# Optimization experiments

Measured on AMD Instinct MI355X. Metric: run time of the kernel, lower is better.

The kernel has to match this reference:

```python
import jax, jax.numpy as jnp
import numpy as np

N = 50000          # nodes
E = 800000         # edges (avg degree 16)
D = 128            # feature dim
MSG_EPS = 1e-7     # GENConv eps added to relu(msg)
SM_EPS = 1e-16     # pyg softmax denominator eps
BN_EPS = 1e-5
LN_EPS = 1e-5


def setup_inputs() -> dict:
    key = jax.random.key(0)
    ks = jax.random.split(key, 6)
    x = jax.random.normal(ks[0], (N, D), dtype=jnp.float32)
    edge_index = jax.random.randint(ks[1], (2, E), 0, N, dtype=jnp.int32)
    t = jnp.array(1.0, dtype=jnp.float32)
    W1 = jax.random.normal(ks[2], (D, 2 * D), dtype=jnp.float32) / np.sqrt(D).astype(np.float32)
    b1 = jnp.zeros((2 * D,), jnp.float32)
    bn_gamma = jnp.ones((2 * D,), jnp.float32)
    bn_beta = jnp.zeros((2 * D,), jnp.float32)
    W2 = jax.random.normal(ks[3], (2 * D, D), dtype=jnp.float32) / np.sqrt(2 * D).astype(np.float32)
    b2 = jnp.zeros((D,), jnp.float32)
    ln_gamma = jnp.ones((D,), jnp.float32)
    ln_beta = jnp.zeros((D,), jnp.float32)
    return {"x": x, "edge_index": edge_index, "t": t, "W1": W1, "b1": b1,
            "bn_gamma": bn_gamma, "bn_beta": bn_beta, "W2": W2, "b2": b2,
            "ln_gamma": ln_gamma, "ln_beta": ln_beta}


def reference(x, edge_index, t, W1, b1, bn_gamma, bn_beta, W2, b2, ln_gamma, ln_beta):
    src, dst = edge_index[0], edge_index[1]
    # --- GENConv message: relu(x_j) + eps  -> [E, D]
    msg = jax.nn.relu(x[src]) + MSG_EPS
    # --- softmax aggregation over incoming edges per dst node, per feature
    logits = t * msg                                            # [E, D]
    seg_max = jax.ops.segment_max(logits, dst, num_segments=N)  # [N, D]
    seg_max = jnp.where(jnp.isfinite(seg_max), seg_max, 0.0)    # empty segments -> 0
    ex = jnp.exp(logits - seg_max[dst])                         # [E, D]
    denom = jax.ops.segment_sum(ex, dst, num_segments=N)        # [N, D]
    alpha = ex / (denom[dst] + SM_EPS)                          # [E, D]
    agg = jax.ops.segment_sum(alpha * msg, dst, num_segments=N) # [N, D]
    # --- GENConv update: MLP(agg + x), MLP = Lin(D,2D)->BN->ReLU->Lin(2D,D)
    h = agg + x
    h = h @ W1 + b1                                             # [N, 2D]
    mu = jnp.mean(h, axis=0)
    var = jnp.var(h, axis=0)
    h = (h - mu) * jax.lax.rsqrt(var + BN_EPS) * bn_gamma + bn_beta
    h = jax.nn.relu(h)
    h = h @ W2 + b2                                             # [N, D]
    # --- LayerNorm -> ReLU -> (dropout p=0 noop) -> residual
    mu2 = jnp.mean(h, axis=-1, keepdims=True)
    var2 = jnp.mean(jnp.square(h - mu2), axis=-1, keepdims=True)
    h = (h - mu2) * jax.lax.rsqrt(var2 + LN_EPS) * ln_gamma + ln_beta
    h = jax.nn.relu(h)
    return x + h
```

## Files before the change

kernel.cpp:

```cpp
#include <hip/hip_runtime.h>

#define D 128
#define D2 256
#define BSH 6
#define BNODES 64
#define NBMAX 1024
#define CAP 1280
#define PCHUNK 4096

typedef __attribute__((ext_vector_type(8))) short short8;
typedef __attribute__((ext_vector_type(4))) float f32x4;

__device__ inline unsigned short f2b(float f) {
  unsigned u = __float_as_uint(f);
  unsigned r = (u + 0x7FFFu + ((u >> 16) & 1u)) >> 16;
  return (unsigned short)r;
}
__device__ inline float b2f(unsigned short h) {
  return __uint_as_float(((unsigned)h) << 16);
}

__global__ void convert_w_kernel(const float* __restrict__ W1,
                                 const float* __restrict__ W2,
                                 unsigned short* __restrict__ W1f,
                                 unsigned short* __restrict__ W2f) {
  int idx = blockIdx.x * 256 + threadIdx.x;
  if (idx < 32768) {
    int k = idx >> 8, n = idx & 255;
    int t = n >> 4, m16 = n & 15;
    int kk = k >> 5, quad = (k >> 3) & 3, j = k & 7;
    W1f[(((t * 4 + kk) * 64 + quad * 16 + m16) << 3) + j] = f2b(W1[idx]);
  } else {
    int i = idx - 32768;
    int k = i >> 7, n = i & 127;
    int t = n >> 4, m16 = n & 15;
    int kk = k >> 5, quad = (k >> 3) & 3, j = k & 7;
    W2f[(((t * 8 + kk) * 64 + quad * 16 + m16) << 3) + j] = f2b(W2[i]);
  }
}

__global__ void mb_kernel(const float* __restrict__ x, unsigned short* __restrict__ mb,
                          int total4) {
  int i = blockIdx.x * 256 + threadIdx.x;
  if (i >= total4) return;
  float4 v = reinterpret_cast<const float4*>(x)[i];
  unsigned lo = (unsigned)f2b(fmaxf(v.x, 0.f) + 1e-7f) |
                ((unsigned)f2b(fmaxf(v.y, 0.f) + 1e-7f) << 16);
  unsigned hi = (unsigned)f2b(fmaxf(v.z, 0.f) + 1e-7f) |
                ((unsigned)f2b(fmaxf(v.w, 0.f) + 1e-7f) << 16);
  reinterpret_cast<uint2*>(mb)[i] = make_uint2(lo, hi);
}

__global__ __launch_bounds__(256) void part_kernel(const int* __restrict__ ei,
                                                   int* __restrict__ cursor,
                                                   unsigned* __restrict__ pairbuf,
                                                   int E, int nb) {
  __shared__ int cnt[NBMAX];
  __shared__ int base[NBMAX];
  int tid = threadIdx.x;
  int c0 = blockIdx.x * PCHUNK;
  int nE = min(PCHUNK, E - c0);
  for (int i = tid; i < nb; i += 256) cnt[i] = 0;
  __syncthreads();
  for (int j = tid; j < nE; j += 256) {
    int dst = ei[E + c0 + j];
    atomicAdd(&cnt[dst >> BSH], 1);
  }
  __syncthreads();
  for (int i = tid; i < nb; i += 256) {
    int c = cnt[i];
    base[i] = (c > 0) ? atomicAdd(&cursor[i], c) : 0;
    cnt[i] = 0;
  }
  __syncthreads();
  for (int j = tid; j < nE; j += 256) {
    int e = c0 + j;
    int dst = ei[E + e];
    int src = ei[e];
    int b = dst >> BSH;
    int r = base[b] + atomicAdd(&cnt[b], 1);
    if (r < CAP)
      pairbuf[(size_t)b * CAP + r] =
          (unsigned)src | ((unsigned)(dst & (BNODES - 1)) << 16);
  }
}

__global__ __launch_bounds__(512) void agg2_kernel(const float* __restrict__ x,
                                                   const unsigned short* __restrict__ mb,
                                                   const unsigned* __restrict__ pairbuf,
                                                   const int* __restrict__ cursor,
                                                   const float* __restrict__ tptr,
                                                   unsigned short* __restrict__ h0b, int N) {
  __shared__ unsigned spair[CAP];
  __shared__ unsigned short ssrc[CAP];
  __shared__ int cnt[BNODES], off[BNODES], run[BNODES];
  int b = blockIdx.x;
  int tid = threadIdx.x;
  int Eb = min(cursor[b], CAP);
  if (tid < BNODES) { cnt[tid] = 0; run[tid] = 0; }
  __syncthreads();
  for (int j = tid; j < Eb; j += 512) {
    unsigned p = pairbuf[(size_t)b * CAP + j];
    spair[j] = p;
    atomicAdd(&cnt[p >> 16], 1);
  }
  __syncthreads();
  if (tid < 64) {
    int v = cnt[tid];
    int s = v;
#pragma unroll
    for (int st = 1; st < 64; st <<= 1) {
      int u = __shfl_up(s, st, 64);
      if (tid >= st) s += u;
    }
    off[tid] = s - v;
  }
  __syncthreads();
  for (int j = tid; j < Eb; j += 512) {
    unsigned p = spair[j];
    int dl = p >> 16;
    int r = atomicAdd(&run[dl], 1);
    ssrc[off[dl] + r] = (unsigned short)(p & 0xffffu);
  }
  __syncthreads();

  int w = tid >> 6;
  int l = tid & 63;
  float t = tptr[0];
  const unsigned short* mbc = mb + 2 * l;
  for (int ln = w; ln < BNODES; ln += 8) {
    int n = (b << BSH) + ln;
    if (n >= N) continue;
    int s0 = off[ln];
    int dn = cnt[ln];
    float den0 = 0.f, num0 = 0.f, den1 = 0.f, num1 = 0.f;
    int j = 0;
    for (; j + 8 <= dn; j += 8) {
      unsigned uu[8];
#pragma unroll
      for (int q = 0; q < 8; ++q) {
        int aq = ssrc[s0 + j + q];
        uu[q] = *reinterpret_cast<const unsigned*>(mbc + ((size_t)aq << 7));
      }
#pragma unroll
      for (int q = 0; q < 8; ++q) {
        float m0 = b2f((unsigned short)(uu[q] & 0xffffu));
        float m1 = b2f((unsigned short)(uu[q] >> 16));
        float e0 = __expf(t * m0);
        float e1 = __expf(t * m1);
        den0 += e0; num0 += e0 * m0;
        den1 += e1; num1 += e1 * m1;
      }
    }
    for (; j < dn; ++j) {
      int aq = ssrc[s0 + j];
      unsigned u = *reinterpret_cast<const unsigned*>(mbc + ((size_t)aq << 7));
      float m0 = b2f((unsigned short)(u & 0xffffu));
      float m1 = b2f((unsigned short)(u >> 16));
      float e0 = __expf(t * m0);
      float e1 = __expf(t * m1);
      den0 += e0; num0 += e0 * m0;
      den1 += e1; num1 += e1 * m1;
    }
    size_t idx = ((size_t)n << 7) + 2 * l;
    float2 xv = *reinterpret_cast<const float2*>(x + idx);
    float v0 = num0 / (den0 + 1e-16f) + xv.x;
    float v1 = num1 / (den1 + 1e-16f) + xv.y;
    *reinterpret_cast<unsigned*>(h0b + idx) =
        (unsigned)f2b(v0) | ((unsigned)f2b(v1) << 16);
  }
}

__global__ __launch_bounds__(256) void gemm1_mfma(
    const unsigned short* __restrict__ h0b, const unsigned short* __restrict__ W1f,
    const float* __restrict__ b1, unsigned short* __restrict__ h1b,
    float* __restrict__ bnsum, float* __restrict__ bnsumsq, int M) {
  int tid = threadIdx.x;
  int w = tid >> 6;
  int l = tid & 63;
  int m16 = l & 15;
  int quad = l >> 4;
  int r0 = blockIdx.x * 64;

  f32x4 acc[4][4];
#pragma unroll
  for (int rt = 0; rt < 4; ++rt)
#pragma unroll
    for (int ct = 0; ct < 4; ++ct) acc[rt][ct] = (f32x4){0.f, 0.f, 0.f, 0.f};

#pragma unroll
  for (int kk = 0; kk < 4; ++kk) {
    short8 bfr[4];
#pragma unroll
    for (int ct = 0; ct < 4; ++ct)
      bfr[ct] = *reinterpret_cast<const short8*>(
          W1f + ((((w * 4 + ct) * 4 + kk) * 64 + l) << 3));
    short8 a[4];
#pragma unroll
    for (int rt = 0; rt < 4; ++rt) {
      int row = min(r0 + rt * 16 + m16, M - 1);
      a[rt] = *reinterpret_cast<const short8*>(h0b + (size_t)row * D + kk * 32 + quad * 8);
    }
#pragma unroll
    for (int rt = 0; rt < 4; ++rt)
#pragma unroll
      for (int ct = 0; ct < 4; ++ct)
        acc[rt][ct] = __builtin_amdgcn_mfma_f32_16x16x32_bf16(a[rt], bfr[ct], acc[rt][ct], 0, 0, 0);
  }

#pragma unroll
  for (int ct = 0; ct < 4; ++ct) {
    int col = w * 64 + ct * 16 + m16;
    float bv = b1[col];
    float cs = 0.f, cq = 0.f;
#pragma unroll
    for (int rt = 0; rt < 4; ++rt) {
      int rowb = r0 + rt * 16 + quad * 4;
#pragma unroll
      for (int reg = 0; reg < 4; ++reg) {
        int row = rowb + reg;
        float val = acc[rt][ct][reg] + bv;
        if (row < M) {
          cs += val;
          cq += val * val;
          h1b[(size_t)row * D2 + col] = f2b(val);
        }
      }
    }
    cs += __shfl_xor(cs, 16, 64);
    cs += __shfl_xor(cs, 32, 64);
    cq += __shfl_xor(cq, 16, 64);
    cq += __shfl_xor(cq, 32, 64);
    if (quad == 0) {
      atomicAdd(&bnsum[col], cs);
      atomicAdd(&bnsumsq[col], cq);
    }
  }
}

__global__ void bnfinal_kernel(const float* __restrict__ bnsum,
                               const float* __restrict__ bnsumsq,
                               const float* __restrict__ gamma,
                               const float* __restrict__ beta,
                               float* __restrict__ scale,
                               float* __restrict__ shift, int M) {
  int c = threadIdx.x;
  float invM = 1.f / (float)M;
  float mu = bnsum[c] * invM;
  float var = bnsumsq[c] * invM - mu * mu;
  float sc = gamma[c] * rsqrtf(var + 1e-5f);
  scale[c] = sc;
  shift[c] = beta[c] - mu * sc;
}

__global__ __launch_bounds__(256) void gemm2_mfma(
    const unsigned short* __restrict__ h1b, const unsigned short* __restrict__ W2f,
    const float* __restrict__ b2, const float* __restrict__ bnscale,
    const float* __restrict__ bnshift, const float* __restrict__ lng,
    const float* __restrict__ lnb, const float* __restrict__ x,
    float* __restrict__ out, int M) {
  __shared__ float lnp[128][2], lnp2[128][2];
  int tid = threadIdx.x;
  int w = tid >> 6;
  int l = tid & 63;
  int m16 = l & 15;
  int quad = l >> 4;
  int rb = w >> 1, cb = w & 1;
  int r00 = blockIdx.x * 128;

  f32x4 acc[4][4];
#pragma unroll
  for (int rt = 0; rt < 4; ++rt)
#pragma unroll
    for (int ct = 0; ct < 4; ++ct) acc[rt][ct] = (f32x4){0.f, 0.f, 0.f, 0.f};

#pragma unroll
  for (int kk = 0; kk < 8; ++kk) {
    int c0 = kk * 32 + quad * 8;
    f32x4 sc0 = *reinterpret_cast<const f32x4*>(bnscale + c0);
    f32x4 sc1 = *reinterpret_cast<const f32x4*>(bnscale + c0 + 4);
    f32x4 sh0 = *reinterpret_cast<const f32x4*>(bnshift + c0);
    f32x4 sh1 = *reinterpret_cast<const f32x4*>(bnshift + c0 + 4);
    short8 a[4];
#pragma unroll
    for (int rt = 0; rt < 4; ++rt) {
      int row = min(r00 + rb * 64 + rt * 16 + m16, M - 1);
      short8 raw = *reinterpret_cast<const short8*>(h1b + (size_t)row * D2 + kk * 32 + quad * 8);
#pragma unroll
      for (int j = 0; j < 4; ++j) {
        a[rt][j] = (short)f2b(fmaxf(b2f((unsigned short)raw[j]) * sc0[j] + sh0[j], 0.f));
        a[rt][j + 4] = (short)f2b(fmaxf(b2f((unsigned short)raw[j + 4]) * sc1[j] + sh1[j], 0.f));
      }
    }
    short8 bfr[4];
#pragma unroll
    for (int ct = 0; ct < 4; ++ct)
      bfr[ct] = *reinterpret_cast<const short8*>(
          W2f + ((((cb * 4 + ct) * 8 + kk) * 64 + l) << 3));
#pragma unroll
    for (int rt = 0; rt < 4; ++rt)
#pragma unroll
      for (int ct = 0; ct < 4; ++ct)
        acc[rt][ct] = __builtin_amdgcn_mfma_f32_16x16x32_bf16(a[rt], bfr[ct], acc[rt][ct], 0, 0, 0);
  }

  float b2v[4], lgv[4], lbv[4];
#pragma unroll
  for (int ct = 0; ct < 4; ++ct) {
    int col = cb * 64 + ct * 16 + m16;
    b2v[ct] = b2[col];
    lgv[ct] = lng[col];
    lbv[ct] = lnb[col];
  }

#pragma unroll
  for (int rt = 0; rt < 4; ++rt) {
#pragma unroll
    for (int reg = 0; reg < 4; ++reg) {
      float s = 0.f, s2 = 0.f;
#pragma unroll
      for (int ct = 0; ct < 4; ++ct) {
        float v = acc[rt][ct][reg] + b2v[ct];
        s += v;
        s2 += v * v;
      }
#pragma unroll
      for (int msk = 1; msk < 16; msk <<= 1) {
        s += __shfl_xor(s, msk, 64);
        s2 += __shfl_xor(s2, msk, 64);
      }
      if (m16 == 0) {
        int rl = rb * 64 + rt * 16 + quad * 4 + reg;
        lnp[rl][cb] = s;
        lnp2[rl][cb] = s2;
      }
    }
  }
  __syncthreads();

#pragma unroll
  for (int rt = 0; rt < 4; ++rt) {
#pragma unroll
    for (int reg = 0; reg < 4; ++reg) {
      int rl = rb * 64 + rt * 16 + quad * 4 + reg;
      int row = r00 + rl;
      float s = lnp[rl][0] + lnp[rl][1];
      float s2 = lnp2[rl][0] + lnp2[rl][1];
      float mu = s * (1.f / 128.f);
      float var = s2 * (1.f / 128.f) - mu * mu;
      float inv = rsqrtf(var + 1e-5f);
      if (row < M) {
#pragma unroll
        for (int ct = 0; ct < 4; ++ct) {
          int col = cb * 64 + ct * 16 + m16;
          float v = acc[rt][ct][reg] + b2v[ct];
          float h = fmaxf((v - mu) * inv * lgv[ct] + lbv[ct], 0.f);
          out[(size_t)row * D + col] = x[(size_t)row * D + col] + h;
        }
      }
    }
  }
}

extern "C" void kernel_launch(void* const* d_in, const int* in_sizes, int n_in,
                              void* d_out, int out_size, void* d_ws, size_t ws_size,
                              hipStream_t stream) {
  const float* x   = (const float*)d_in[0];
  const int*   ei  = (const int*)d_in[1];
  const float* t   = (const float*)d_in[2];
  const float* W1  = (const float*)d_in[3];
  const float* b1  = (const float*)d_in[4];
  const float* bng = (const float*)d_in[5];
  const float* bnb = (const float*)d_in[6];
  const float* W2  = (const float*)d_in[7];
  const float* b2  = (const float*)d_in[8];
  const float* lng = (const float*)d_in[9];
  const float* lnb = (const float*)d_in[10];
  float* out = (float*)d_out;

  int N = in_sizes[0] / D;
  int E = in_sizes[1] / 2;
  size_t nd = (size_t)N * D;
  int nb = (N + BNODES - 1) >> BSH;

  unsigned short* mb  = (unsigned short*)d_ws;
  unsigned short* h0b = mb + nd;
  unsigned short* h1b = h0b + nd;
  unsigned short* W1f = h1b + 2 * nd;
  unsigned short* W2f = W1f + 32768;
  float* bnsum   = (float*)(W2f + 32768);
  float* bnsumsq = bnsum + D2;
  float* bnscale = bnsumsq + D2;
  float* bnshift = bnscale + D2;
  int* cursor = (int*)(bnshift + D2);
  unsigned* pairbuf = (unsigned*)(cursor + NBMAX);

  hipMemsetAsync(bnsum, 0, (4 * D2 + NBMAX) * sizeof(int), stream);

  convert_w_kernel<<<256, 256, 0, stream>>>(W1, W2, W1f, W2f);
  int total4 = (int)(nd / 4);
  mb_kernel<<<(total4 + 255) / 256, 256, 0, stream>>>(x, mb, total4);

  part_kernel<<<(E + PCHUNK - 1) / PCHUNK, 256, 0, stream>>>(ei, cursor, pairbuf, E, nb);
  agg2_kernel<<<nb, 512, 0, stream>>>(x, mb, pairbuf, cursor, t, h0b, N);

  gemm1_mfma<<<(N + 63) / 64, 256, 0, stream>>>(h0b, W1f, b1, h1b, bnsum, bnsumsq, N);
  bnfinal_kernel<<<1, 256, 0, stream>>>(bnsum, bnsumsq, bng, bnb, bnscale, bnshift, N);
  gemm2_mfma<<<(N + 127) / 128, 256, 0, stream>>>(h1b, W2f, b2, bnscale, bnshift, lng, lnb, x, out, N);
}
```

Baseline: 242.3 us.

## Shrink aggregation buckets, stage GEMM1 output via LDS, split BN apply kernel

Aggregation buckets shrink from 64 to 32 nodes, with 256-thread blocks and a 32-wide scan, which doubles the block count and raises occupancy. GEMM1 drops the b1 bias, since batch norm cancels it, and stages its bf16 tile in shared memory so rows are written with wide coalesced stores instead of scattered 2-byte stores. The BN scale/shift/ReLU step moves out of GEMM2's inner loop into a separate elementwise kernel that writes a normalized copy h1c. That adds an extra read and write of a 2*N*D bf16 buffer plus one more launch in exchange for a simpler GEMM2 A-load path.

```diff
diff --git a/kernel.cpp b/kernel.cpp
--- a/kernel.cpp
+++ b/kernel.cpp
@@ -2,10 +2,10 @@
 
 #define D 128
 #define D2 256
-#define BSH 6
-#define BNODES 64
-#define NBMAX 1024
-#define CAP 1280
+#define BSH 5
+#define BNODES 32
+#define NBMAX 2048
+#define CAP 640
 #define PCHUNK 4096
 
 typedef __attribute__((ext_vector_type(8))) short short8;
@@ -85,7 +85,7 @@
   }
 }
 
-__global__ __launch_bounds__(512) void agg2_kernel(const float* __restrict__ x,
+__global__ __launch_bounds__(256) void agg2_kernel(const float* __restrict__ x,
                                                    const unsigned short* __restrict__ mb,
                                                    const unsigned* __restrict__ pairbuf,
                                                    const int* __restrict__ cursor,
@@ -99,24 +99,24 @@
   int Eb = min(cursor[b], CAP);
   if (tid < BNODES) { cnt[tid] = 0; run[tid] = 0; }
   __syncthreads();
-  for (int j = tid; j < Eb; j += 512) {
+  for (int j = tid; j < Eb; j += 256) {
     unsigned p = pairbuf[(size_t)b * CAP + j];
     spair[j] = p;
     atomicAdd(&cnt[p >> 16], 1);
   }
   __syncthreads();
-  if (tid < 64) {
+  if (tid < BNODES) {
     int v = cnt[tid];
     int s = v;
 #pragma unroll
-    for (int st = 1; st < 64; st <<= 1) {
-      int u = __shfl_up(s, st, 64);
-      if (tid >= st) s += u;
+    for (int st = 1; st < 32; st <<= 1) {
+      int u = __shfl_up(s, st, 32);
+      if ((tid & 31) >= st) s += u;
     }
     off[tid] = s - v;
   }
   __syncthreads();
-  for (int j = tid; j < Eb; j += 512) {
+  for (int j = tid; j < Eb; j += 256) {
     unsigned p = spair[j];
     int dl = p >> 16;
     int r = atomicAdd(&run[dl], 1);
@@ -128,7 +128,7 @@
   int l = tid & 63;
   float t = tptr[0];
   const unsigned short* mbc = mb + 2 * l;
-  for (int ln = w; ln < BNODES; ln += 8) {
+  for (int ln = w; ln < BNODES; ln += 4) {
     int n = (b << BSH) + ln;
     if (n >= N) continue;
     int s0 = off[ln];
@@ -173,8 +173,9 @@
 
 __global__ __launch_bounds__(256) void gemm1_mfma(
     const unsigned short* __restrict__ h0b, const unsigned short* __restrict__ W1f,
-    const float* __restrict__ b1, unsigned short* __restrict__ h1b,
+    unsigned short* __restrict__ h1b,
     float* __restrict__ bnsum, float* __restrict__ bnsumsq, int M) {
+  __shared__ unsigned short lt[4][64][72];
   int tid = threadIdx.x;
   int w = tid >> 6;
   int l = tid & 63;
@@ -211,20 +212,18 @@
 #pragma unroll
   for (int ct = 0; ct < 4; ++ct) {
     int col = w * 64 + ct * 16 + m16;
-    float bv = b1[col];
     float cs = 0.f, cq = 0.f;
 #pragma unroll
     for (int rt = 0; rt < 4; ++rt) {
-      int rowb = r0 + rt * 16 + quad * 4;
+      int rloc = rt * 16 + quad * 4;
 #pragma unroll
       for (int reg = 0; reg < 4; ++reg) {
-        int row = rowb + reg;
-        float val = acc[rt][ct][reg] + bv;
-        if (row < M) {
+        float val = acc[rt][ct][reg];
+        if (r0 + rloc + reg < M) {
           cs += val;
           cq += val * val;
-          h1b[(size_t)row * D2 + col] = f2b(val);
         }
+        lt[w][rloc + reg][ct * 16 + m16] = f2b(val);
       }
     }
     cs += __shfl_xor(cs, 16, 64);
@@ -235,6 +234,16 @@
       atomicAdd(&bnsum[col], cs);
       atomicAdd(&bnsumsq[col], cq);
     }
+  }
+
+  int row = r0 + l;
+  if (row < M) {
+    const unsigned short* src = &lt[w][l][0];
+    unsigned short* dst = h1b + (size_t)row * D2 + w * 64;
+#pragma unroll
+    for (int j = 0; j < 8; ++j)
+      *reinterpret_cast<short8*>(dst + j * 8) =
+          *reinterpret_cast<const short8*>(src + j * 8);
   }
 }
 
@@ -253,10 +262,39 @@
   shift[c] = beta[c] - mu * sc;
 }
 
+__global__ __launch_bounds__(256) void bnapply_kernel(
+    const unsigned short* __restrict__ h1b, const float* __restrict__ scale,
+    const float* __restrict__ shift, unsigned short* __restrict__ h1c, int total8) {
+  int i = blockIdx.x * 256 + threadIdx.x;
+  if (i >= total8) return;
+  int c0 = (i << 3) & 255;
+  f32x4 sc0 = *reinterpret_cast<const f32x4*>(scale + c0);
+  f32x4 sc1 = *reinterpret_cast<const f32x4*>(scale + c0 + 4);
+  f32x4 sh0 = *reinterpret_cast<const f32x4*>(shift + c0);
+  f32x4 sh1 = *reinterpret_cast<const f32x4*>(shift + c0 + 4);
+  uint4 raw = reinterpret_cast<const uint4*>(h1b)[i];
+  unsigned words[4] = {raw.x, raw.y, raw.z, raw.w};
+  uint4 o;
+  unsigned ow[4];
+#pragma unroll
+  for (int p = 0; p < 2; ++p) {
+    f32x4 sc = p ? sc1 : sc0;
+    f32x4 sh = p ? sh1 : sh0;
+#pragma unroll
+    for (int q = 0; q < 2; ++q) {
+      unsigned u = words[p * 2 + q];
+      float v0 = fmaxf(b2f((unsigned short)(u & 0xffffu)) * sc[q * 2] + sh[q * 2], 0.f);
+      float v1 = fmaxf(b2f((unsigned short)(u >> 16)) * sc[q * 2 + 1] + sh[q * 2 + 1], 0.f);
+      ow[p * 2 + q] = (unsigned)f2b(v0) | ((unsigned)f2b(v1) << 16);
+    }
+  }
+  o.x = ow[0]; o.y = ow[1]; o.z = ow[2]; o.w = ow[3];
+  reinterpret_cast<uint4*>(h1c)[i] = o;
+}
+
 __global__ __launch_bounds__(256) void gemm2_mfma(
-    const unsigned short* __restrict__ h1b, const unsigned short* __restrict__ W2f,
-    const float* __restrict__ b2, const float* __restrict__ bnscale,
-    const float* __restrict__ bnshift, const float* __restrict__ lng,
+    const unsigned short* __restrict__ h1c, const unsigned short* __restrict__ W2f,
+    const float* __restrict__ b2, const float* __restrict__ lng,
     const float* __restrict__ lnb, const float* __restrict__ x,
     float* __restrict__ out, int M) {
   __shared__ float lnp[128][2], lnp2[128][2];
@@ -276,21 +314,11 @@
 
 #pragma unroll
   for (int kk = 0; kk < 8; ++kk) {
-    int c0 = kk * 32 + quad * 8;
-    f32x4 sc0 = *reinterpret_cast<const f32x4*>(bnscale + c0);
-    f32x4 sc1 = *reinterpret_cast<const f32x4*>(bnscale + c0 + 4);
-    f32x4 sh0 = *reinterpret_cast<const f32x4*>(bnshift + c0);
-    f32x4 sh1 = *reinterpret_cast<const f32x4*>(bnshift + c0 + 4);
     short8 a[4];
 #pragma unroll
     for (int rt = 0; rt < 4; ++rt) {
       int row = min(r00 + rb * 64 + rt * 16 + m16, M - 1);
-      short8 raw = *reinterpret_cast<const short8*>(h1b + (size_t)row * D2 + kk * 32 + quad * 8);
-#pragma unroll
-      for (int j = 0; j < 4; ++j) {
-        a[rt][j] = (short)f2b(fmaxf(b2f((unsigned short)raw[j]) * sc0[j] + sh0[j], 0.f));
-        a[rt][j + 4] = (short)f2b(fmaxf(b2f((unsigned short)raw[j + 4]) * sc1[j] + sh1[j], 0.f));
-      }
+      a[rt] = *reinterpret_cast<const short8*>(h1c + (size_t)row * D2 + kk * 32 + quad * 8);
     }
     short8 bfr[4];
 #pragma unroll
@@ -369,7 +397,6 @@
   const int*   ei  = (const int*)d_in[1];
   const float* t   = (const float*)d_in[2];
   const float* W1  = (const float*)d_in[3];
-  const float* b1  = (const float*)d_in[4];
   const float* bng = (const float*)d_in[5];
   const float* bnb = (const float*)d_in[6];
   const float* W2  = (const float*)d_in[7];
@@ -386,7 +413,8 @@
   unsigned short* mb  = (unsigned short*)d_ws;
   unsigned short* h0b = mb + nd;
   unsigned short* h1b = h0b + nd;
-  unsigned short* W1f = h1b + 2 * nd;
+  unsigned short* h1c = h1b + 2 * nd;
+  unsigned short* W1f = h1c + 2 * nd;
   unsigned short* W2f = W1f + 32768;
   float* bnsum   = (float*)(W2f + 32768);
   float* bnsumsq = bnsum + D2;
@@ -402,9 +430,11 @@
   mb_kernel<<<(total4 + 255) / 256, 256, 0, stream>>>(x, mb, total4);
 
   part_kernel<<<(E + PCHUNK - 1) / PCHUNK, 256, 0, stream>>>(ei, cursor, pairbuf, E, nb);
-  agg2_kernel<<<nb, 512, 0, stream>>>(x, mb, pairbuf, cursor, t, h0b, N);
-
-  gemm1_mfma<<<(N + 63) / 64, 256, 0, stream>>>(h0b, W1f, b1, h1b, bnsum, bnsumsq, N);
+  agg2_kernel<<<nb, 256, 0, stream>>>(x, mb, pairbuf, cursor, t, h0b, N);
+
+  gemm1_mfma<<<(N + 63) / 64, 256, 0, stream>>>(h0b, W1f, h1b, bnsum, bnsumsq, N);
   bnfinal_kernel<<<1, 256, 0, stream>>>(bnsum, bnsumsq, bng, bnb, bnscale, bnshift, N);
-  gemm2_mfma<<<(N + 127) / 128, 256, 0, stream>>>(h1b, W2f, b2, bnscale, bnshift, lng, lnb, x, out, N);
-}
+  int total8 = (int)(2 * nd / 8);
+  bnapply_kernel<<<(total8 + 255) / 256, 256, 0, stream>>>(h1b, bnscale, bnshift, h1c, total8);
+  gemm2_mfma<<<(N + 127) / 128, 256, 0, stream>>>(h1c, W2f, b2, lng, lnb, x, out, N);
+}
```

New measurement: 231.2 us. -4.6%, faster.
